# Performance work log

Hardware: AMD Instinct MI355X
Metric: run time of the kernel (lower is better)

The kernel has to match this reference:

```python
import jax, jax.numpy as jnp
import numpy as np

MAX_DISP = 64  # init kwarg max_disp; feature_similarity='correlation'


def setup_inputs() -> dict:
    key = jax.random.key(0)
    k1, k2 = jax.random.split(key)
    shape = (8, 160, 320, 128)  # (b, h, w, c)
    left = jax.random.normal(k1, shape, dtype=jnp.float32)
    right = jax.random.normal(k2, shape, dtype=jnp.float32)
    return {"left_feature": left, "right_feature": right}


def reference(left_feature, right_feature):
    # Faithful to CostVolume.__call__ with feature_similarity='correlation':
    # cost[b,h,j,i] = mean_c( left[b,h,j,c] * right[b,h,j-i,c] ) for j >= i, else 0.
    b, h, w, c = left_feature.shape
    widx = jnp.arange(w)  # (w,)
    slices = []
    for i in range(MAX_DISP):  # fixed hyperparameter unroll, not a data dim
        # roll brings right[..., j-i, :] to position j along width; wrapped
        # positions j < i are masked to zero (original leaves them at init 0).
        corr = jnp.mean(left_feature * jnp.roll(right_feature, i, axis=2), axis=3)  # (b,h,w)
        corr = jnp.where(widx >= i, corr, jnp.zeros((), corr.dtype))
        slices.append(corr)
    return jnp.stack(slices, axis=-1)  # (b, h, w, max_disp)
```

## Files before the change

### kernel.cpp

```cpp
#include <hip/hip_runtime.h>

#define W 320

typedef __attribute__((ext_vector_type(8))) short   short8;
typedef __attribute__((ext_vector_type(4))) float   floatx4;

__device__ __forceinline__ unsigned int f2bf(float f) {
    unsigned int u = __float_as_uint(f);
    u += 0x7FFFu + ((u >> 16) & 1u);
    return u >> 16;
}

#define LOAD8(buf, base, toff) do {                                         \
    const float* p_ = (base) + (size_t)(toff) * 2048;                       \
    _Pragma("unroll")                                                       \
    for (int q_ = 0; q_ < 4; ++q_) {                                        \
        buf[2*q_]   = *(const floatx4*)(p_ + q_*32);                        \
        buf[2*q_+1] = *(const floatx4*)(p_ + q_*32 + 4);                    \
    } } while (0)

#define CONV8(dst, buf) do {                                                \
    _Pragma("unroll")                                                       \
    for (int q_ = 0; q_ < 4; ++q_) {                                        \
        short8 x_;                                                          \
        x_[0] = (short)f2bf(buf[2*q_].x);   x_[1] = (short)f2bf(buf[2*q_].y);   \
        x_[2] = (short)f2bf(buf[2*q_].z);   x_[3] = (short)f2bf(buf[2*q_].w);   \
        x_[4] = (short)f2bf(buf[2*q_+1].x); x_[5] = (short)f2bf(buf[2*q_+1].y); \
        x_[6] = (short)f2bf(buf[2*q_+1].z); x_[7] = (short)f2bf(buf[2*q_+1].w); \
        (dst)[q_] = x_;                                                     \
    } } while (0)

__global__ __launch_bounds__(256, 2)
void cost_volume_kernel(const float* __restrict__ Lg,
                        const float* __restrict__ Rg,
                        float* __restrict__ out) {
    const int lin = blockIdx.x;
    const int bh  = (lin & 7) * 160 + (lin >> 3);
    const int tid = threadIdx.x;
    const int w    = tid >> 6;
    const int lane = tid & 63;
    const int col  = lane & 15;
    const int quad = lane >> 4;

    const float* Rb = Rg + ((size_t)bh * W + col) * 128 + quad * 8;
    const float* Lb = Lg + ((size_t)bh * W + col) * 128 + quad * 8;
    float* obase = out + (size_t)bh * W * 64;

    floatx4 rbufA[8], rbufB[8], abuf[8];
    short8  Bf[5][4];
    short8  Af[4];

    const int T0 = 5 * w;

    if (T0 >= 4) LOAD8(rbufA, Rb, T0 - 4);
    if (T0 >= 3) LOAD8(rbufB, Rb, T0 - 3);
    LOAD8(abuf, Lb, T0);
    if (T0 >= 4) CONV8(Bf[1], rbufA);
    if (T0 >= 2) LOAD8(rbufA, Rb, T0 - 2);
    if (T0 >= 3) CONV8(Bf[2], rbufB);
    if (T0 >= 1) LOAD8(rbufB, Rb, T0 - 1);
    if (T0 >= 2) CONV8(Bf[3], rbufA);
    LOAD8(rbufA, Rb, T0);
    if (T0 >= 1) CONV8(Bf[4], rbufB);
    CONV8(Bf[0], rbufA);

    #pragma unroll
    for (int u = 0; u < 5; ++u) {
        CONV8(Af, abuf);

        if (u < 4) {
            LOAD8(abuf,  Lb, T0 + u + 1);
            LOAD8(rbufA, Rb, T0 + u + 1);
        }

        floatx4 acc[5];
        #pragma unroll
        for (int v = 0; v < 5; ++v) {
            acc[v].x = 0.f; acc[v].y = 0.f; acc[v].z = 0.f; acc[v].w = 0.f;
        }

        #pragma unroll
        for (int v = 0; v < 5; ++v) {
            if (T0 + u + v >= 4) {
                #pragma unroll
                for (int ks = 0; ks < 4; ++ks) {
                    acc[v] = __builtin_amdgcn_mfma_f32_16x16x32_bf16(
                        Af[ks], Bf[(u + 1 + v) % 5][ks], acc[v], 0, 0, 0);
                }
            }
        }

        float* orow = obase + (size_t)(T0 + u) * 16 * 64;
        #pragma unroll
        for (int v = 0; v < 5; ++v) {
            #pragma unroll
            for (int r = 0; r < 4; ++r) {
                const int m = quad * 4 + r;
                const int i = 64 - 16 * v + m - col;
                const bool ok = (v == 0) ? (m < col) : (v == 4) ? (m >= col) : true;
                if (ok) orow[(size_t)m * 64 + i] = acc[v][r] * 0.0078125f;
            }
        }

        if (u < 4) CONV8(Bf[(u + 1) % 5], rbufA);
    }
}

extern "C" void kernel_launch(void* const* d_in, const int* in_sizes, int n_in,
                              void* d_out, int out_size, void* d_ws, size_t ws_size,
                              hipStream_t stream) {
    const float* L = (const float*)d_in[0];
    const float* R = (const float*)d_in[1];
    float* out = (float*)d_out;
    dim3 grid(8 * 160);
    cost_volume_kernel<<<grid, 256, 0, stream>>>(L, R, out);
}
```

Measured before the change: 443.1 us.

## Split each row across five blocks, one 16-column tile per wave

Each block used to handle a whole (b,h) row, with every wave walking five 16-column tiles and reusing converted right-feature fragments across tiles. Now the grid is five times larger and each wave computes exactly one tile, loading the five needed right tiles directly. Launch bounds are raised to 3 blocks per CU. The aim is more parallelism and occupancy and less register pressure for hiding memory latency, at the cost of reloading and reconverting right-feature data about five times instead of once per tile.

```diff
diff --git a/kernel.cpp b/kernel.cpp
--- a/kernel.cpp
+++ b/kernel.cpp
@@ -30,79 +30,65 @@
         (dst)[q_] = x_;                                                     \
     } } while (0)
 
-__global__ __launch_bounds__(256, 2)
+#define MFMA4(accv) do {                                                    \
+    _Pragma("unroll")                                                       \
+    for (int ks_ = 0; ks_ < 4; ++ks_)                                       \
+        accv = __builtin_amdgcn_mfma_f32_16x16x32_bf16(Af[ks_], Bt[ks_],    \
+                                                       accv, 0, 0, 0);     \
+    } while (0)
+
+__global__ __launch_bounds__(256, 3)
 void cost_volume_kernel(const float* __restrict__ Lg,
                         const float* __restrict__ Rg,
                         float* __restrict__ out) {
-    const int lin = blockIdx.x;
-    const int bh  = (lin & 7) * 160 + (lin >> 3);
-    const int tid = threadIdx.x;
-    const int w    = tid >> 6;
-    const int lane = tid & 63;
+    const int lin  = blockIdx.x;
+    const int work = (lin & 7) * 800 + (lin >> 3);
+    const int bh   = work / 5;
+    const int grp  = work - bh * 5;
+
+    const int wave = threadIdx.x >> 6;
+    const int t    = grp * 4 + wave;
+    const int lane = threadIdx.x & 63;
     const int col  = lane & 15;
     const int quad = lane >> 4;
 
     const float* Rb = Rg + ((size_t)bh * W + col) * 128 + quad * 8;
     const float* Lb = Lg + ((size_t)bh * W + col) * 128 + quad * 8;
-    float* obase = out + (size_t)bh * W * 64;
 
-    floatx4 rbufA[8], rbufB[8], abuf[8];
-    short8  Bf[5][4];
-    short8  Af[4];
+    floatx4 bufA[8], bufB[8], bufC[8];
+    short8  Af[4], Bt[4];
 
-    const int T0 = 5 * w;
+    LOAD8(bufC, Lb, t);
+    if (t >= 4) LOAD8(bufA, Rb, t - 4);
+    if (t >= 3) LOAD8(bufB, Rb, t - 3);
 
-    if (T0 >= 4) LOAD8(rbufA, Rb, T0 - 4);
-    if (T0 >= 3) LOAD8(rbufB, Rb, T0 - 3);
-    LOAD8(abuf, Lb, T0);
-    if (T0 >= 4) CONV8(Bf[1], rbufA);
-    if (T0 >= 2) LOAD8(rbufA, Rb, T0 - 2);
-    if (T0 >= 3) CONV8(Bf[2], rbufB);
-    if (T0 >= 1) LOAD8(rbufB, Rb, T0 - 1);
-    if (T0 >= 2) CONV8(Bf[3], rbufA);
-    LOAD8(rbufA, Rb, T0);
-    if (T0 >= 1) CONV8(Bf[4], rbufB);
-    CONV8(Bf[0], rbufA);
+    CONV8(Af, bufC);
+    if (t >= 2) LOAD8(bufC, Rb, t - 2);
 
+    floatx4 acc[5];
     #pragma unroll
-    for (int u = 0; u < 5; ++u) {
-        CONV8(Af, abuf);
+    for (int v = 0; v < 5; ++v) {
+        acc[v].x = 0.f; acc[v].y = 0.f; acc[v].z = 0.f; acc[v].w = 0.f;
+    }
 
-        if (u < 4) {
-            LOAD8(abuf,  Lb, T0 + u + 1);
-            LOAD8(rbufA, Rb, T0 + u + 1);
+    if (t >= 4) { CONV8(Bt, bufA); MFMA4(acc[0]); }
+    if (t >= 1) LOAD8(bufA, Rb, t - 1);
+    if (t >= 3) { CONV8(Bt, bufB); MFMA4(acc[1]); }
+    LOAD8(bufB, Rb, t);
+    if (t >= 2) { CONV8(Bt, bufC); MFMA4(acc[2]); }
+    if (t >= 1) { CONV8(Bt, bufA); MFMA4(acc[3]); }
+    CONV8(Bt, bufB); MFMA4(acc[4]);
+
+    float* orow = out + ((size_t)bh * W + (size_t)t * 16) * 64;
+    #pragma unroll
+    for (int v = 0; v < 5; ++v) {
+        #pragma unroll
+        for (int r = 0; r < 4; ++r) {
+            const int m = quad * 4 + r;
+            const int i = 64 - 16 * v + m - col;
+            const bool ok = (v == 0) ? (m < col) : (v == 4) ? (m >= col) : true;
+            if (ok) orow[(size_t)m * 64 + i] = acc[v][r] * 0.0078125f;
         }
-
-        floatx4 acc[5];
-        #pragma unroll
-        for (int v = 0; v < 5; ++v) {
-            acc[v].x = 0.f; acc[v].y = 0.f; acc[v].z = 0.f; acc[v].w = 0.f;
-        }
-
-        #pragma unroll
-        for (int v = 0; v < 5; ++v) {
-            if (T0 + u + v >= 4) {
-                #pragma unroll
-                for (int ks = 0; ks < 4; ++ks) {
-                    acc[v] = __builtin_amdgcn_mfma_f32_16x16x32_bf16(
-                        Af[ks], Bf[(u + 1 + v) % 5][ks], acc[v], 0, 0, 0);
-                }
-            }
-        }
-
-        float* orow = obase + (size_t)(T0 + u) * 16 * 64;
-        #pragma unroll
-        for (int v = 0; v < 5; ++v) {
-            #pragma unroll
-            for (int r = 0; r < 4; ++r) {
-                const int m = quad * 4 + r;
-                const int i = 64 - 16 * v + m - col;
-                const bool ok = (v == 0) ? (m < col) : (v == 4) ? (m >= col) : true;
-                if (ok) orow[(size_t)m * 64 + i] = acc[v][r] * 0.0078125f;
-            }
-        }
-
-        if (u < 4) CONV8(Bf[(u + 1) % 5], rbufA);
     }
 }
 
@@ -112,6 +98,6 @@
     const float* L = (const float*)d_in[0];
     const float* R = (const float*)d_in[1];
     float* out = (float*)d_out;
-    dim3 grid(8 * 160);
+    dim3 grid(8 * 160 * 5);
     cost_volume_kernel<<<grid, 256, 0, stream>>>(L, R, out);
 }
```

After: 461.1 us. 1.04x slower.
